# Performance work log

Hardware: AMD Instinct MI355X
Metric: run time of the kernel (lower is better)

Reference implementation:

```python
import jax, jax.numpy as jnp
import numpy as np

NUM_ITERATIONS = 5
NUM_TERMS = 3  # (degree + 1) // 2 with degree = 5
INITIAL_SCALE = 1.1


def setup_inputs() -> dict:
    key = jax.random.key(0)
    k1, k2 = jax.random.split(key)
    X = jax.random.normal(k1, (64, 1024, 1024), dtype=jnp.float32)
    coefficients = jnp.array([3.4445, -4.7750, 2.0315], dtype=jnp.float32)
    return {"X": X, "coefficients": coefficients}


def reference(X, coefficients):
    # Normalize each matrix to Frobenius norm INITIAL_SCALE
    fro = jnp.sqrt(jnp.sum(X * X, axis=(-2, -1), keepdims=True))
    X = X / fro * INITIAL_SCALE
    for _ in range(NUM_ITERATIONS):
        # XTX = X^T X, shape [B, M, M]
        XTX = jnp.einsum('bji,bjk->bik', X, X)
        term = X
        acc = coefficients[0] * X
        for i in range(1, NUM_TERMS):
            term = jnp.einsum('bij,bjk->bik', term, XTX)  # X (X^T X)^i
            acc = acc + coefficients[i] * term
        X = acc
    return X
```

## Files before the change

### kernel.cpp

```cpp
#include <hip/hip_runtime.h>
#include <hip/hip_bf16.h>
#include <stdint.h>

typedef float f32x4 __attribute__((ext_vector_type(4)));
typedef short bf16x8 __attribute__((ext_vector_type(8)));

#define LDW 1024
#define BATCH_SH 20

__device__ __forceinline__ float b2f(__hip_bfloat16 h) { return __bfloat162float(h); }
__device__ __forceinline__ __hip_bfloat16 f2b(float f) { return __float2bfloat16(f); }

__device__ __forceinline__ void gload16(const void* g, void* l) {
  __builtin_amdgcn_global_load_lds((const __attribute__((address_space(1))) void*)g,
                                   (__attribute__((address_space(3))) void*)l,
                                   16, 0, 0);
}

__global__ void k_partial(const float* __restrict__ xin, float* __restrict__ partials) {
  const int b = blockIdx.y, ch = blockIdx.x, t = threadIdx.x;
  const size_t base = ((size_t)b << BATCH_SH) + (size_t)ch * 16384;
  float s = 0.f;
#pragma unroll
  for (int i = 0; i < 16; ++i) {
    f32x4 v = *reinterpret_cast<const f32x4*>(xin + base + (size_t)(i * 256 + t) * 4);
    s += v[0] * v[0] + v[1] * v[1] + v[2] * v[2] + v[3] * v[3];
  }
#pragma unroll
  for (int off = 32; off; off >>= 1) s += __shfl_down(s, off);
  __shared__ float red[4];
  if ((t & 63) == 0) red[t >> 6] = s;
  __syncthreads();
  if (t == 0) partials[b * 64 + ch] = red[0] + red[1] + red[2] + red[3];
}

__global__ void k_scalesplit(const float* __restrict__ xin, const float* __restrict__ partials,
                             __hip_bfloat16* __restrict__ Xh, __hip_bfloat16* __restrict__ Xl,
                             __hip_bfloat16* __restrict__ XTh, __hip_bfloat16* __restrict__ XTl) {
  __shared__ float tile[64][65];
  const int b = blockIdx.z, tm = blockIdx.y, tn = blockIdx.x;
  const size_t boff = (size_t)b << BATCH_SH;
  const int t = threadIdx.x, lr0 = t >> 6, lc = t & 63;
  float q = partials[b * 64 + (t & 63)];
#pragma unroll
  for (int off = 32; off; off >>= 1) q += __shfl_down(q, off);
  q = __shfl(q, 0);
  const float s = 1.1f / sqrtf(q);
#pragma unroll
  for (int p = 0; p < 16; ++p) {
    const int lr = p * 4 + lr0;
    const size_t idx = boff + (size_t)(tm * 64 + lr) * LDW + tn * 64 + lc;
    const float v = xin[idx] * s;
    __hip_bfloat16 h = f2b(v);
    Xh[idx] = h;
    Xl[idx] = f2b(v - b2f(h));
    tile[lr][lc] = v;
  }
  __syncthreads();
#pragma unroll
  for (int p = 0; p < 16; ++p) {
    const int lr = p * 4 + lr0;
    const float v = tile[lc][lr];
    const size_t idx = boff + (size_t)(tn * 64 + lr) * LDW + tm * 64 + lc;
    __hip_bfloat16 h = f2b(v);
    XTh[idx] = h;
    XTl[idx] = f2b(v - b2f(h));
  }
}


#define SEGPTRS(S)                                                                        \
  const int seg_ = (S) >> 4, k0_ = ((S) & 15) << 6;                                       \
  const __hip_bfloat16* pa_ = seg_ == 0 ? pa0 : seg_ == 1 ? pa1 : pa2;                    \
  const __hip_bfloat16* pb_ = seg_ == 0 ? pb0 : seg_ == 1 ? pb1 : pb2;

#define STAGE_GL(DB, S)                                                                   \
  {                                                                                       \
    SEGPTRS(S)                                                                            \
    char* lb_ = smem + (DB) * 65536;                                                      \
    _Pragma("unroll") for (int it_ = 0; it_ < 4; ++it_) {                                 \
      const int r_ = it_ * 64 + w * 8 + (l >> 3);                                         \
      const int kx_ = k0_ + (((l & 7) ^ (l >> 3)) << 3);                                  \
      gload16(pa_ + boff + (size_t)(rowA + r_) * LDW + kx_,                               \
              lb_ + (it_ * 64 + w * 8) * 128 + l * 16);                                   \
      gload16(pb_ + boff + (size_t)(rowB + r_) * LDW + kx_,                               \
              lb_ + 32768 + (it_ * 64 + w * 8) * 128 + l * 16);                           \
    }                                                                                     \
  }

#define MFMA_PHASE(KK, BASE)                                                              \
  {                                                                                       \
    bf16x8 av[8], bv[4];                                                                  \
    _Pragma("unroll") for (int mi_ = 0; mi_ < 8; ++mi_)                                   \
        av[mi_] = *reinterpret_cast<const bf16x8*>(smem + (BASE) + offA[KK][mi_]);        \
    _Pragma("unroll") for (int ni_ = 0; ni_ < 4; ++ni_)                                   \
        bv[ni_] = *reinterpret_cast<const bf16x8*>(smem + (BASE) + offB[KK][ni_]);        \
    __builtin_amdgcn_s_setprio(1);                                                        \
    _Pragma("unroll") for (int mi_ = 0; mi_ < 8; ++mi_)                                   \
        _Pragma("unroll") for (int ni_ = 0; ni_ < 4; ++ni_)                               \
            acc[mi_][ni_] = __builtin_amdgcn_mfma_f32_16x16x32_bf16(                      \
                av[mi_], bv[ni_], acc[mi_][ni_], 0, 0, 0);                                \
    __builtin_amdgcn_s_setprio(0);                                                        \
  }

template <int MODE>
__global__ __launch_bounds__(512, 2) void k_gemm(
    const __hip_bfloat16* __restrict__ pa0, const __hip_bfloat16* __restrict__ pa1,
    const __hip_bfloat16* __restrict__ pa2, const __hip_bfloat16* __restrict__ pb0,
    const __hip_bfloat16* __restrict__ pb1, const __hip_bfloat16* __restrict__ pb2,
    __hip_bfloat16* oh, __hip_bfloat16* ol,
    __hip_bfloat16* oth, __hip_bfloat16* otl,
    float* __restrict__ of,
    const __hip_bfloat16* __restrict__ eh, const __hip_bfloat16* __restrict__ el,
    const float* __restrict__ coef) {
  __shared__ __align__(16) char smem[131072];
  const int t = threadIdx.x;
  const int w = t >> 6, l = t & 63;
  const int wr = w >> 2, wc = w & 3;

  const int nwg = gridDim.x, q = nwg >> 3, r8 = nwg & 7;
  const int xcd = blockIdx.x & 7, o = blockIdx.x >> 3;
  const int wgid = (xcd < r8 ? xcd * (q + 1) : r8 * (q + 1) + (xcd - r8) * q) + o;

  int bat, tm, tn;
  if constexpr (MODE == 3) {
    bat = wgid >> 4;
    const int tile = wgid & 15;
    tm = tile >> 2; tn = tile & 3;
  } else {
    bat = (int)((unsigned)wgid / 10u);
    const int tile = wgid - bat * 10;
    tm = (tile < 4) ? 0 : (tile < 7) ? 1 : (tile < 9) ? 2 : 3;
    tn = (tile < 4) ? tile : (tile < 7) ? (tile - 3) : (tile < 9) ? (tile - 5) : 3;
  }
  const size_t boff = (size_t)bat << BATCH_SH;
  const int rowA = tm * 256, rowB = tn * 256;

  f32x4 acc[8][4];
#pragma unroll
  for (int i = 0; i < 8; ++i)
#pragma unroll
    for (int j = 0; j < 4; ++j) acc[i][j] = (f32x4){0.f, 0.f, 0.f, 0.f};

  int offA[2][8], offB[2][4];
#pragma unroll
  for (int kk = 0; kk < 2; ++kk) {
    const int g = kk * 4 + (l >> 4);
#pragma unroll
    for (int mi = 0; mi < 8; ++mi) {
      const int rA = wr * 128 + mi * 16 + (l & 15);
      offA[kk][mi] = rA * 128 + ((g ^ (rA & 7)) << 4);
    }
#pragma unroll
    for (int ni = 0; ni < 4; ++ni) {
      const int rB = wc * 64 + ni * 16 + (l & 15);
      offB[kk][ni] = 32768 + rB * 128 + ((g ^ (rB & 7)) << 4);
    }
  }

  STAGE_GL(0, 0);
  asm volatile("s_waitcnt vmcnt(0)" ::: "memory");
  __builtin_amdgcn_sched_barrier(0);
  __builtin_amdgcn_s_barrier();
  __builtin_amdgcn_sched_barrier(0);

  for (int s = 0; s < 48; ++s) {
    const int base = (s & 1) * 65536;
    if (s + 1 < 48) STAGE_GL((s & 1) ^ 1, s + 1);
    __builtin_amdgcn_sched_barrier(0);
    MFMA_PHASE(0, base);
    MFMA_PHASE(1, base);
    asm volatile("s_waitcnt vmcnt(0) lgkmcnt(0)" ::: "memory");
    __builtin_amdgcn_sched_barrier(0);
    __builtin_amdgcn_s_barrier();
    __builtin_amdgcn_sched_barrier(0);
  }

  float c0 = 0.f, c1 = 0.f, c2 = 0.f;
  if constexpr (MODE == 2) { c0 = coef[0]; c1 = coef[1]; c2 = coef[2]; }
  const int r0 = tm * 256 + wr * 128 + ((l >> 4) << 2);
  const int cb = tn * 256 + wc * 64 + (l & 15);
#pragma unroll
  for (int mi = 0; mi < 8; ++mi) {
#pragma unroll
    for (int ni = 0; ni < 4; ++ni) {
      const int ccol = cb + ni * 16;
#pragma unroll
      for (int j = 0; j < 4; ++j) {
        const int rrow = r0 + mi * 16 + j;
        const size_t idx = boff + (size_t)rrow * LDW + ccol;
        float v = acc[mi][ni][j];
        if constexpr (MODE == 2)
          v = c2 * v + c1 * (b2f(eh[idx]) + b2f(el[idx])) + (rrow == ccol ? c0 : 0.f);
        __hip_bfloat16 h = f2b(v);
        __hip_bfloat16 lo = f2b(v - b2f(h));
        if constexpr (MODE == 3) {
          if (oh) { oh[idx] = h; ol[idx] = lo; }
          if (of) of[idx] = v;
        } else {
          oh[idx] = h; ol[idx] = lo;
          if (tm != tn) {
            const size_t tix = boff + (size_t)ccol * LDW + rrow;
            oth[tix] = h; otl[tix] = lo;
          }
        }
      }
    }
  }

  if constexpr (MODE == 3) {
    if (oth) {
      unsigned* tlds = reinterpret_cast<unsigned*>(smem);
      unsigned short* pth = reinterpret_cast<unsigned short*>(oth);
      unsigned short* ptl = reinterpret_cast<unsigned short*>(otl);
#pragma unroll
      for (int h2 = 0; h2 < 2; ++h2) {
        __builtin_amdgcn_s_barrier();
        if ((wc >> 1) == h2) {
#pragma unroll
          for (int mi = 0; mi < 8; ++mi) {
#pragma unroll
            for (int ni = 0; ni < 4; ++ni) {
              const int cl = (wc & 1) * 64 + ni * 16 + (l & 15);
#pragma unroll
              for (int j = 0; j < 4; ++j) {
                const int rr = wr * 128 + ((l >> 4) << 2) + mi * 16 + j;
                const float v = acc[mi][ni][j];
                const __hip_bfloat16 hh = f2b(v);
                const __hip_bfloat16 lo = f2b(v - b2f(hh));
                const unsigned pk = (unsigned)(*(const unsigned short*)&hh) |
                                    ((unsigned)(*(const unsigned short*)&lo) << 16);
                tlds[rr * 128 + (cl ^ ((rr >> 1) & 31))] = pk;
              }
            }
          }
        }
        __builtin_amdgcn_s_barrier();
#pragma unroll
        for (int i = 0; i < 16; ++i) {
          const int trow = w * 16 + i;
          const size_t obase =
              boff + (size_t)(tn * 256 + h2 * 128 + trow) * LDW + tm * 256;
#pragma unroll
          for (int c = 0; c < 2; ++c) {
            const int e0 = (c * 64 + l) * 2;
            const int m = (e0 >> 1) & 31;
            const unsigned p0 = tlds[e0 * 128 + (trow ^ m)];
            const unsigned p1 = tlds[(e0 + 1) * 128 + (trow ^ m)];
            *reinterpret_cast<unsigned*>(pth + obase + e0) =
                (p0 & 0xffffu) | (p1 << 16);
            *reinterpret_cast<unsigned*>(ptl + obase + e0) =
                (p0 >> 16) | (p1 & 0xffff0000u);
          }
        }
      }
    }
  }
}

extern "C" void kernel_launch(void* const* d_in, const int* in_sizes, int n_in,
                              void* d_out, int out_size, void* d_ws, size_t ws_size,
                              hipStream_t stream) {
  (void)in_sizes; (void)n_in; (void)out_size;
  const float* xin = (const float*)d_in[0];
  const float* coef = (const float*)d_in[1];
  float* xout = (float*)d_out;

  int CH = 64;
  while (CH > 1 && ((size_t)CH * 16u * 1024u * 1024u + 65536u) > ws_size) CH >>= 1;

  const size_t nE = (size_t)CH << BATCH_SH;
  __hip_bfloat16* P0h = (__hip_bfloat16*)d_ws;
  __hip_bfloat16* P0l = P0h + nE;
  __hip_bfloat16* P1h = P0l + nE;
  __hip_bfloat16* P1l = P1h + nE;
  __hip_bfloat16* P2h = P1l + nE;
  __hip_bfloat16* P2l = P2h + nE;
  __hip_bfloat16* XTh = P2l + nE;
  __hip_bfloat16* XTl = XTh + nE;
  float* partials = (float*)(XTl + nE);

  for (int c = 0; c < 64; c += CH) {
    const float* xi = xin + ((size_t)c << BATCH_SH);
    float* X = xout + ((size_t)c << BATCH_SH);
    k_partial<<<dim3(64, CH), 256, 0, stream>>>(xi, partials);
    k_scalesplit<<<dim3(16, 16, CH), 256, 0, stream>>>(xi, partials, P0h, P0l, XTh, XTl);

    __hip_bfloat16 *Xh = P0h, *Xl = P0l, *Ah = P1h, *Al = P1l, *Bh = P2h, *Bl = P2l;
    for (int it = 0; it < 5; ++it) {
      k_gemm<1><<<dim3(CH * 10), 512, 0, stream>>>(XTh, XTh, XTl, XTh, XTl, XTh,
                                                   Ah, Al, Ah, Al, nullptr,
                                                   nullptr, nullptr, nullptr);
      k_gemm<2><<<dim3(CH * 10), 512, 0, stream>>>(Ah, Ah, Al, Ah, Al, Ah,
                                                   Bh, Bl, Bh, Bl, nullptr,
                                                   Ah, Al, coef);
      k_gemm<3><<<dim3(CH * 16), 512, 0, stream>>>(Xh, Xh, Xl, Bh, Bl, Bh,
                                                   (it < 4) ? Ah : nullptr,
                                                   (it < 4) ? Al : nullptr,
                                                   (it < 4) ? XTh : nullptr,
                                                   (it < 4) ? XTl : nullptr,
                                                   (it == 4) ? X : nullptr,
                                                   nullptr, nullptr, nullptr);
      __hip_bfloat16 *th = Xh, *tl = Xl;
      Xh = Ah; Xl = Al;
      Ah = Bh; Al = Bl;
      Bh = th; Bl = tl;
    }
  }
}
```

Measured before the change: 7.440 ms.

## Fuse all stages into a persistent megakernel with grid barriers and per-XCD work stealing

Replaces the sequence of norm, scale/split and three GEMM kernel launches per iteration with one persistent kernel of 256 blocks. Stages are separated by atomic grid barriers, and symmetric-GEMM tiles are handed out through per-XCD atomic work-stealing counters. Batches are pinned to XCDs so their data stays in that XCD's L2. This removes launch gaps and tail effects between the 17 launches, but the kernel now runs at one block per CU (launch bounds 512,1), adds spin-barrier overhead, and relies on all 256 blocks being co-resident.

```diff
diff --git a/kernel.cpp b/kernel.cpp
--- a/kernel.cpp
+++ b/kernel.cpp
@@ -7,6 +7,8 @@
 
 #define LDW 1024
 #define BATCH_SH 20
+#define NBLK 256
+#define SCOPE __HIP_MEMORY_SCOPE_AGENT
 
 __device__ __forceinline__ float b2f(__hip_bfloat16 h) { return __bfloat162float(h); }
 __device__ __forceinline__ __hip_bfloat16 f2b(float f) { return __float2bfloat16(f); }
@@ -17,55 +19,19 @@
                                    16, 0, 0);
 }
 
-__global__ void k_partial(const float* __restrict__ xin, float* __restrict__ partials) {
-  const int b = blockIdx.y, ch = blockIdx.x, t = threadIdx.x;
-  const size_t base = ((size_t)b << BATCH_SH) + (size_t)ch * 16384;
-  float s = 0.f;
-#pragma unroll
-  for (int i = 0; i < 16; ++i) {
-    f32x4 v = *reinterpret_cast<const f32x4*>(xin + base + (size_t)(i * 256 + t) * 4);
-    s += v[0] * v[0] + v[1] * v[1] + v[2] * v[2] + v[3] * v[3];
-  }
-#pragma unroll
-  for (int off = 32; off; off >>= 1) s += __shfl_down(s, off);
-  __shared__ float red[4];
-  if ((t & 63) == 0) red[t >> 6] = s;
+__device__ __forceinline__ void grid_bar(int* cnt, int idx) {
   __syncthreads();
-  if (t == 0) partials[b * 64 + ch] = red[0] + red[1] + red[2] + red[3];
-}
-
-__global__ void k_scalesplit(const float* __restrict__ xin, const float* __restrict__ partials,
-                             __hip_bfloat16* __restrict__ Xh, __hip_bfloat16* __restrict__ Xl,
-                             __hip_bfloat16* __restrict__ XTh, __hip_bfloat16* __restrict__ XTl) {
-  __shared__ float tile[64][65];
-  const int b = blockIdx.z, tm = blockIdx.y, tn = blockIdx.x;
-  const size_t boff = (size_t)b << BATCH_SH;
-  const int t = threadIdx.x, lr0 = t >> 6, lc = t & 63;
-  float q = partials[b * 64 + (t & 63)];
-#pragma unroll
-  for (int off = 32; off; off >>= 1) q += __shfl_down(q, off);
-  q = __shfl(q, 0);
-  const float s = 1.1f / sqrtf(q);
-#pragma unroll
-  for (int p = 0; p < 16; ++p) {
-    const int lr = p * 4 + lr0;
-    const size_t idx = boff + (size_t)(tm * 64 + lr) * LDW + tn * 64 + lc;
-    const float v = xin[idx] * s;
-    __hip_bfloat16 h = f2b(v);
-    Xh[idx] = h;
-    Xl[idx] = f2b(v - b2f(h));
-    tile[lr][lc] = v;
+  if (threadIdx.x == 0) {
+    __hip_atomic_fetch_add(cnt, 1, __ATOMIC_ACQ_REL, SCOPE);
+    const int target = idx * NBLK;
+    while (__hip_atomic_load(cnt, __ATOMIC_ACQUIRE, SCOPE) < target)
+      __builtin_amdgcn_s_sleep(2);
   }
   __syncthreads();
-#pragma unroll
-  for (int p = 0; p < 16; ++p) {
-    const int lr = p * 4 + lr0;
-    const float v = tile[lc][lr];
-    const size_t idx = boff + (size_t)(tn * 64 + lr) * LDW + tm * 64 + lc;
-    __hip_bfloat16 h = f2b(v);
-    XTh[idx] = h;
-    XTl[idx] = f2b(v - b2f(h));
-  }
+}
+
+__global__ void k_zero(int* p, int n) {
+  if ((int)threadIdx.x < n) p[threadIdx.x] = 0;
 }
 
 
@@ -103,37 +69,17 @@
     __builtin_amdgcn_s_setprio(0);                                                        \
   }
 
-template <int MODE>
-__global__ __launch_bounds__(512, 2) void k_gemm(
-    const __hip_bfloat16* __restrict__ pa0, const __hip_bfloat16* __restrict__ pa1,
-    const __hip_bfloat16* __restrict__ pa2, const __hip_bfloat16* __restrict__ pb0,
-    const __hip_bfloat16* __restrict__ pb1, const __hip_bfloat16* __restrict__ pb2,
+__device__ __forceinline__ void gemm_tile(
+    const int mode, char* smem, const int t, const size_t boff,
+    const int tm, const int tn,
+    const __hip_bfloat16* pa0, const __hip_bfloat16* pa1, const __hip_bfloat16* pa2,
+    const __hip_bfloat16* pb0, const __hip_bfloat16* pb1, const __hip_bfloat16* pb2,
     __hip_bfloat16* oh, __hip_bfloat16* ol,
-    __hip_bfloat16* oth, __hip_bfloat16* otl,
-    float* __restrict__ of,
-    const __hip_bfloat16* __restrict__ eh, const __hip_bfloat16* __restrict__ el,
-    const float* __restrict__ coef) {
-  __shared__ __align__(16) char smem[131072];
-  const int t = threadIdx.x;
+    __hip_bfloat16* oth, __hip_bfloat16* otl, float* of,
+    const __hip_bfloat16* eh, const __hip_bfloat16* el,
+    const float c0, const float c1, const float c2) {
   const int w = t >> 6, l = t & 63;
   const int wr = w >> 2, wc = w & 3;
-
-  const int nwg = gridDim.x, q = nwg >> 3, r8 = nwg & 7;
-  const int xcd = blockIdx.x & 7, o = blockIdx.x >> 3;
-  const int wgid = (xcd < r8 ? xcd * (q + 1) : r8 * (q + 1) + (xcd - r8) * q) + o;
-
-  int bat, tm, tn;
-  if constexpr (MODE == 3) {
-    bat = wgid >> 4;
-    const int tile = wgid & 15;
-    tm = tile >> 2; tn = tile & 3;
-  } else {
-    bat = (int)((unsigned)wgid / 10u);
-    const int tile = wgid - bat * 10;
-    tm = (tile < 4) ? 0 : (tile < 7) ? 1 : (tile < 9) ? 2 : 3;
-    tn = (tile < 4) ? tile : (tile < 7) ? (tile - 3) : (tile < 9) ? (tile - 5) : 3;
-  }
-  const size_t boff = (size_t)bat << BATCH_SH;
   const int rowA = tm * 256, rowB = tn * 256;
 
   f32x4 acc[8][4];
@@ -176,8 +122,6 @@
     __builtin_amdgcn_sched_barrier(0);
   }
 
-  float c0 = 0.f, c1 = 0.f, c2 = 0.f;
-  if constexpr (MODE == 2) { c0 = coef[0]; c1 = coef[1]; c2 = coef[2]; }
   const int r0 = tm * 256 + wr * 128 + ((l >> 4) << 2);
   const int cb = tn * 256 + wc * 64 + (l & 15);
 #pragma unroll
@@ -190,11 +134,11 @@
         const int rrow = r0 + mi * 16 + j;
         const size_t idx = boff + (size_t)rrow * LDW + ccol;
         float v = acc[mi][ni][j];
-        if constexpr (MODE == 2)
+        if (mode == 2)
           v = c2 * v + c1 * (b2f(eh[idx]) + b2f(el[idx])) + (rrow == ccol ? c0 : 0.f);
         __hip_bfloat16 h = f2b(v);
         __hip_bfloat16 lo = f2b(v - b2f(h));
-        if constexpr (MODE == 3) {
+        if (mode == 3) {
           if (oh) { oh[idx] = h; ol[idx] = lo; }
           if (of) of[idx] = v;
         } else {
@@ -208,53 +152,198 @@
     }
   }
 
-  if constexpr (MODE == 3) {
-    if (oth) {
-      unsigned* tlds = reinterpret_cast<unsigned*>(smem);
-      unsigned short* pth = reinterpret_cast<unsigned short*>(oth);
-      unsigned short* ptl = reinterpret_cast<unsigned short*>(otl);
-#pragma unroll
-      for (int h2 = 0; h2 < 2; ++h2) {
-        __builtin_amdgcn_s_barrier();
-        if ((wc >> 1) == h2) {
-#pragma unroll
-          for (int mi = 0; mi < 8; ++mi) {
-#pragma unroll
-            for (int ni = 0; ni < 4; ++ni) {
-              const int cl = (wc & 1) * 64 + ni * 16 + (l & 15);
-#pragma unroll
-              for (int j = 0; j < 4; ++j) {
-                const int rr = wr * 128 + ((l >> 4) << 2) + mi * 16 + j;
-                const float v = acc[mi][ni][j];
-                const __hip_bfloat16 hh = f2b(v);
-                const __hip_bfloat16 lo = f2b(v - b2f(hh));
-                const unsigned pk = (unsigned)(*(const unsigned short*)&hh) |
-                                    ((unsigned)(*(const unsigned short*)&lo) << 16);
-                tlds[rr * 128 + (cl ^ ((rr >> 1) & 31))] = pk;
-              }
+  if (mode == 3 && oth) {
+    unsigned* tlds = reinterpret_cast<unsigned*>(smem);
+    unsigned short* pth = reinterpret_cast<unsigned short*>(oth);
+    unsigned short* ptl = reinterpret_cast<unsigned short*>(otl);
+#pragma unroll
+    for (int h2 = 0; h2 < 2; ++h2) {
+      __builtin_amdgcn_s_barrier();
+      if ((wc >> 1) == h2) {
+#pragma unroll
+        for (int mi = 0; mi < 8; ++mi) {
+#pragma unroll
+          for (int ni = 0; ni < 4; ++ni) {
+            const int cl = (wc & 1) * 64 + ni * 16 + (l & 15);
+#pragma unroll
+            for (int j = 0; j < 4; ++j) {
+              const int rr = wr * 128 + ((l >> 4) << 2) + mi * 16 + j;
+              const float v = acc[mi][ni][j];
+              const __hip_bfloat16 hh = f2b(v);
+              const __hip_bfloat16 lo = f2b(v - b2f(hh));
+              const unsigned pk = (unsigned)(*(const unsigned short*)&hh) |
+                                  ((unsigned)(*(const unsigned short*)&lo) << 16);
+              tlds[rr * 128 + (cl ^ ((rr >> 1) & 31))] = pk;
             }
           }
         }
-        __builtin_amdgcn_s_barrier();
-#pragma unroll
-        for (int i = 0; i < 16; ++i) {
-          const int trow = w * 16 + i;
-          const size_t obase =
-              boff + (size_t)(tn * 256 + h2 * 128 + trow) * LDW + tm * 256;
-#pragma unroll
-          for (int c = 0; c < 2; ++c) {
-            const int e0 = (c * 64 + l) * 2;
-            const int m = (e0 >> 1) & 31;
-            const unsigned p0 = tlds[e0 * 128 + (trow ^ m)];
-            const unsigned p1 = tlds[(e0 + 1) * 128 + (trow ^ m)];
-            *reinterpret_cast<unsigned*>(pth + obase + e0) =
-                (p0 & 0xffffu) | (p1 << 16);
-            *reinterpret_cast<unsigned*>(ptl + obase + e0) =
-                (p0 >> 16) | (p1 & 0xffff0000u);
-          }
+      }
+      __builtin_amdgcn_s_barrier();
+#pragma unroll
+      for (int i = 0; i < 16; ++i) {
+        const int trow = w * 16 + i;
+        const size_t obase = boff + (size_t)(tn * 256 + h2 * 128 + trow) * LDW + tm * 256;
+#pragma unroll
+        for (int c = 0; c < 2; ++c) {
+          const int e0 = (c * 64 + l) * 2;
+          const int m = (e0 >> 1) & 31;
+          const unsigned p0 = tlds[e0 * 128 + (trow ^ m)];
+          const unsigned p1 = tlds[(e0 + 1) * 128 + (trow ^ m)];
+          *reinterpret_cast<unsigned*>(pth + obase + e0) = (p0 & 0xffffu) | (p1 << 16);
+          *reinterpret_cast<unsigned*>(ptl + obase + e0) = (p0 >> 16) | (p1 & 0xffff0000u);
         }
       }
     }
+    __syncthreads();
+  }
+}
+
+__global__ __launch_bounds__(512, 1) void k_mega(
+    const float* __restrict__ xin, const float* __restrict__ coef,
+    float* __restrict__ xout,
+    __hip_bfloat16* P0h, __hip_bfloat16* P0l,
+    __hip_bfloat16* P1h, __hip_bfloat16* P1l,
+    __hip_bfloat16* P2h, __hip_bfloat16* P2l,
+    __hip_bfloat16* XTh, __hip_bfloat16* XTl,
+    float* __restrict__ partials, int* cnt, int* steal, const int CH) {
+  __shared__ __align__(16) char smem[131072];
+  __shared__ int jslot;
+  const int t = threadIdx.x, bid = blockIdx.x;
+  const int xcd = bid & 7, lid = bid >> 3;
+  const int bpx = CH >> 3;
+  int bar = 0;
+
+  {
+    const int per = CH * 8;
+    float* red = reinterpret_cast<float*>(smem);
+    for (int j = lid; j < per; j += 32) {
+      const int f = xcd * per + j;
+      const int b = f >> 6, ch = f & 63;
+      const size_t base = ((size_t)b << BATCH_SH) + (size_t)ch * 16384;
+      float s = 0.f;
+#pragma unroll
+      for (int i = 0; i < 8; ++i) {
+        f32x4 v = *reinterpret_cast<const f32x4*>(xin + base + (size_t)(i * 512 + t) * 4);
+        s += v[0] * v[0] + v[1] * v[1] + v[2] * v[2] + v[3] * v[3];
+      }
+#pragma unroll
+      for (int off = 32; off; off >>= 1) s += __shfl_down(s, off);
+      if ((t & 63) == 0) red[t >> 6] = s;
+      __syncthreads();
+      if (t == 0) {
+        float tot = 0.f;
+#pragma unroll
+        for (int i = 0; i < 8; ++i) tot += red[i];
+        partials[f] = tot;
+      }
+      __syncthreads();
+    }
+  }
+  grid_bar(cnt, ++bar);
+
+  {
+    const int per = CH * 32;
+    float* tile = reinterpret_cast<float*>(smem);
+    const int lr0 = t >> 6, lc = t & 63;
+    for (int j = lid; j < per; j += 32) {
+      const int f = xcd * per + j;
+      const int b = f >> 8, t256 = f & 255;
+      const int tmm = t256 >> 4, tnn = t256 & 15;
+      const size_t boff = (size_t)b << BATCH_SH;
+      float q = partials[b * 64 + (t & 63)];
+#pragma unroll
+      for (int off = 32; off; off >>= 1) q += __shfl_down(q, off);
+      q = __shfl(q, 0);
+      const float sc = 1.1f / sqrtf(q);
+#pragma unroll
+      for (int p = 0; p < 8; ++p) {
+        const int lr = p * 8 + lr0;
+        const size_t idx = boff + (size_t)(tmm * 64 + lr) * LDW + tnn * 64 + lc;
+        const float v = xin[idx] * sc;
+        __hip_bfloat16 h = f2b(v);
+        P0h[idx] = h;
+        P0l[idx] = f2b(v - b2f(h));
+        tile[lr * 65 + lc] = v;
+      }
+      __syncthreads();
+#pragma unroll
+      for (int p = 0; p < 8; ++p) {
+        const int lr = p * 8 + lr0;
+        const float v = tile[lc * 65 + lr];
+        const size_t idx = boff + (size_t)(tnn * 64 + lr) * LDW + tmm * 64 + lc;
+        __hip_bfloat16 h = f2b(v);
+        XTh[idx] = h;
+        XTl[idx] = f2b(v - b2f(h));
+      }
+      __syncthreads();
+    }
+  }
+  grid_bar(cnt, ++bar);
+
+  const float c0 = coef[0], c1 = coef[1], c2 = coef[2];
+
+  for (int it = 0; it < 5; ++it) {
+    const int rX = it % 3, rA = (it + 1) % 3, rB = (it + 2) % 3;
+    __hip_bfloat16* Xh = rX == 0 ? P0h : rX == 1 ? P1h : P2h;
+    __hip_bfloat16* Xl = rX == 0 ? P0l : rX == 1 ? P1l : P2l;
+    __hip_bfloat16* Ah = rA == 0 ? P0h : rA == 1 ? P1h : P2h;
+    __hip_bfloat16* Al = rA == 0 ? P0l : rA == 1 ? P1l : P2l;
+    __hip_bfloat16* Bh = rB == 0 ? P0h : rB == 1 ? P1h : P2h;
+    __hip_bfloat16* Bl = rB == 0 ? P0l : rB == 1 ? P1l : P2l;
+
+    {
+      const int NT = (CH * 10) >> 3;
+      int* ctr = steal + (it * 2) * 8 + xcd;
+      for (;;) {
+        if (t == 0) jslot = __hip_atomic_fetch_add(ctr, 1, __ATOMIC_RELAXED, SCOPE);
+        __syncthreads();
+        const int j = jslot;
+        __syncthreads();
+        if (j >= NT) break;
+        const int bat = xcd * bpx + j / 10;
+        const int tl = j - (j / 10) * 10;
+        const int tmm = (tl < 4) ? 0 : (tl < 7) ? 1 : (tl < 9) ? 2 : 3;
+        const int tnn = (tl < 4) ? tl : (tl < 7) ? (tl - 3) : (tl < 9) ? (tl - 5) : 3;
+        gemm_tile(1, smem, t, (size_t)bat << BATCH_SH, tmm, tnn,
+                  XTh, XTh, XTl, XTh, XTl, XTh,
+                  Ah, Al, Ah, Al, nullptr, nullptr, nullptr, 0.f, 0.f, 0.f);
+      }
+    }
+    grid_bar(cnt, ++bar);
+
+    {
+      const int NT = (CH * 10) >> 3;
+      int* ctr = steal + (it * 2 + 1) * 8 + xcd;
+      for (;;) {
+        if (t == 0) jslot = __hip_atomic_fetch_add(ctr, 1, __ATOMIC_RELAXED, SCOPE);
+        __syncthreads();
+        const int j = jslot;
+        __syncthreads();
+        if (j >= NT) break;
+        const int bat = xcd * bpx + j / 10;
+        const int tl = j - (j / 10) * 10;
+        const int tmm = (tl < 4) ? 0 : (tl < 7) ? 1 : (tl < 9) ? 2 : 3;
+        const int tnn = (tl < 4) ? tl : (tl < 7) ? (tl - 3) : (tl < 9) ? (tl - 5) : 3;
+        gemm_tile(2, smem, t, (size_t)bat << BATCH_SH, tmm, tnn,
+                  Ah, Ah, Al, Ah, Al, Ah,
+                  Bh, Bl, Bh, Bl, nullptr, Ah, Al, c0, c1, c2);
+      }
+    }
+    grid_bar(cnt, ++bar);
+
+    {
+      const int NT = CH * 2;
+      for (int j = lid; j < NT; j += 32) {
+        const int bat = xcd * bpx + (j >> 4);
+        const int t16 = j & 15;
+        gemm_tile(3, smem, t, (size_t)bat << BATCH_SH, t16 >> 2, t16 & 3,
+                  Xh, Xh, Xl, Bh, Bl, Bh,
+                  (it < 4) ? Ah : nullptr, (it < 4) ? Al : nullptr,
+                  (it < 4) ? XTh : nullptr, (it < 4) ? XTl : nullptr,
+                  (it == 4) ? xout : nullptr, nullptr, nullptr, 0.f, 0.f, 0.f);
+      }
+    }
+    if (it < 4) grid_bar(cnt, ++bar);
   }
 }
 
@@ -267,7 +356,7 @@
   float* xout = (float*)d_out;
 
   int CH = 64;
-  while (CH > 1 && ((size_t)CH * 16u * 1024u * 1024u + 65536u) > ws_size) CH >>= 1;
+  while (CH > 8 && ((size_t)CH * 16u * 1024u * 1024u + 65536u) > ws_size) CH >>= 1;
 
   const size_t nE = (size_t)CH << BATCH_SH;
   __hip_bfloat16* P0h = (__hip_bfloat16*)d_ws;
@@ -279,32 +368,14 @@
   __hip_bfloat16* XTh = P2l + nE;
   __hip_bfloat16* XTl = XTh + nE;
   float* partials = (float*)(XTl + nE);
+  int* sync_area = (int*)(partials + (size_t)CH * 64);
 
   for (int c = 0; c < 64; c += CH) {
     const float* xi = xin + ((size_t)c << BATCH_SH);
     float* X = xout + ((size_t)c << BATCH_SH);
-    k_partial<<<dim3(64, CH), 256, 0, stream>>>(xi, partials);
-    k_scalesplit<<<dim3(16, 16, CH), 256, 0, stream>>>(xi, partials, P0h, P0l, XTh, XTl);
-
-    __hip_bfloat16 *Xh = P0h, *Xl = P0l, *Ah = P1h, *Al = P1l, *Bh = P2h, *Bl = P2l;
-    for (int it = 0; it < 5; ++it) {
-      k_gemm<1><<<dim3(CH * 10), 512, 0, stream>>>(XTh, XTh, XTl, XTh, XTl, XTh,
-                                                   Ah, Al, Ah, Al, nullptr,
-                                                   nullptr, nullptr, nullptr);
-      k_gemm<2><<<dim3(CH * 10), 512, 0, stream>>>(Ah, Ah, Al, Ah, Al, Ah,
-                                                   Bh, Bl, Bh, Bl, nullptr,
-                                                   Ah, Al, coef);
-      k_gemm<3><<<dim3(CH * 16), 512, 0, stream>>>(Xh, Xh, Xl, Bh, Bl, Bh,
-                                                   (it < 4) ? Ah : nullptr,
-                                                   (it < 4) ? Al : nullptr,
-                                                   (it < 4) ? XTh : nullptr,
-                                                   (it < 4) ? XTl : nullptr,
-                                                   (it == 4) ? X : nullptr,
-                                                   nullptr, nullptr, nullptr);
-      __hip_bfloat16 *th = Xh, *tl = Xl;
-      Xh = Ah; Xl = Al;
-      Ah = Bh; Al = Bl;
-      Bh = th; Bl = tl;
-    }
-  }
-}
+    k_zero<<<dim3(1), 128, 0, stream>>>(sync_area, 81);
+    k_mega<<<dim3(NBLK), 512, 0, stream>>>(xi, coef, X,
+                                           P0h, P0l, P1h, P1l, P2h, P2l, XTh, XTl,
+                                           partials, sync_area, sync_area + 1, CH);
+  }
+}
```

New measurement: 27.74 ms. 273% more time.

## Prefetch two stages ahead and overlap global loads with second MFMA half

Applied to the files above, without the earlier changes.

Restructures the GEMM main loop so that two K-stages are in flight. Each iteration reads the second half's fragments into registers, then issues a barrier so the current buffer can be refilled with stage s+2 while the second MFMA half runs. It waits on vmcnt(8) instead of draining all loads, so global-load latency is hidden more deeply. The cost is more live registers for the extra fragments, plus an additional barrier per iteration.

```diff
diff --git a/kernel.cpp b/kernel.cpp
--- a/kernel.cpp
+++ b/kernel.cpp
@@ -88,20 +88,16 @@
     }                                                                                     \
   }
 
-#define MFMA_PHASE(KK, BASE)                                                              \
-  {                                                                                       \
-    bf16x8 av[8], bv[4];                                                                  \
-    _Pragma("unroll") for (int mi_ = 0; mi_ < 8; ++mi_)                                   \
-        av[mi_] = *reinterpret_cast<const bf16x8*>(smem + (BASE) + offA[KK][mi_]);        \
-    _Pragma("unroll") for (int ni_ = 0; ni_ < 4; ++ni_)                                   \
-        bv[ni_] = *reinterpret_cast<const bf16x8*>(smem + (BASE) + offB[KK][ni_]);        \
-    __builtin_amdgcn_s_setprio(1);                                                        \
-    _Pragma("unroll") for (int mi_ = 0; mi_ < 8; ++mi_)                                   \
-        _Pragma("unroll") for (int ni_ = 0; ni_ < 4; ++ni_)                               \
-            acc[mi_][ni_] = __builtin_amdgcn_mfma_f32_16x16x32_bf16(                      \
-                av[mi_], bv[ni_], acc[mi_][ni_], 0, 0, 0);                                \
-    __builtin_amdgcn_s_setprio(0);                                                        \
-  }
+#define MFMA_CL(AV, BV)                                                                   \
+  __builtin_amdgcn_s_setprio(1);                                                          \
+  _Pragma("unroll") for (int mi_ = 0; mi_ < 8; ++mi_)                                     \
+      _Pragma("unroll") for (int ni_ = 0; ni_ < 4; ++ni_)                                 \
+          acc[mi_][ni_] = __builtin_amdgcn_mfma_f32_16x16x32_bf16(                        \
+              AV[mi_], BV[ni_], acc[mi_][ni_], 0, 0, 0);                                  \
+  __builtin_amdgcn_s_setprio(0);
+
+#define SCB() __builtin_amdgcn_sched_barrier(0)
+#define BAR() __builtin_amdgcn_s_barrier()
 
 template <int MODE>
 __global__ __launch_bounds__(512, 2) void k_gemm(
@@ -159,21 +155,43 @@
   }
 
   STAGE_GL(0, 0);
-  asm volatile("s_waitcnt vmcnt(0)" ::: "memory");
-  __builtin_amdgcn_sched_barrier(0);
-  __builtin_amdgcn_s_barrier();
-  __builtin_amdgcn_sched_barrier(0);
+  STAGE_GL(1, 1);
+  asm volatile("s_waitcnt vmcnt(8)" ::: "memory");
+  SCB();
+  BAR();
+  SCB();
 
   for (int s = 0; s < 48; ++s) {
     const int base = (s & 1) * 65536;
-    if (s + 1 < 48) STAGE_GL((s & 1) ^ 1, s + 1);
-    __builtin_amdgcn_sched_barrier(0);
-    MFMA_PHASE(0, base);
-    MFMA_PHASE(1, base);
-    asm volatile("s_waitcnt vmcnt(0) lgkmcnt(0)" ::: "memory");
-    __builtin_amdgcn_sched_barrier(0);
-    __builtin_amdgcn_s_barrier();
-    __builtin_amdgcn_sched_barrier(0);
+    bf16x8 av0[8], bv0[4], av1[8], bv1[4];
+#pragma unroll
+    for (int i = 0; i < 8; ++i)
+      av0[i] = *reinterpret_cast<const bf16x8*>(smem + base + offA[0][i]);
+#pragma unroll
+    for (int i = 0; i < 4; ++i)
+      bv0[i] = *reinterpret_cast<const bf16x8*>(smem + base + offB[0][i]);
+    MFMA_CL(av0, bv0);
+#pragma unroll
+    for (int i = 0; i < 8; ++i)
+      av1[i] = *reinterpret_cast<const bf16x8*>(smem + base + offA[1][i]);
+#pragma unroll
+    for (int i = 0; i < 4; ++i)
+      bv1[i] = *reinterpret_cast<const bf16x8*>(smem + base + offB[1][i]);
+    asm volatile("s_waitcnt lgkmcnt(0)" ::: "memory");
+    SCB();
+    BAR();
+    SCB();
+    if (s + 2 < 48) STAGE_GL((s & 1), s + 2);
+    SCB();
+    MFMA_CL(av1, bv1);
+    if (s + 2 < 48) {
+      asm volatile("s_waitcnt vmcnt(8)" ::: "memory");
+    } else {
+      asm volatile("s_waitcnt vmcnt(0)" ::: "memory");
+    }
+    SCB();
+    BAR();
+    SCB();
   }
 
   float c0 = 0.f, c1 = 0.f, c2 = 0.f;
```

After: 7.542 ms. Within noise of the previous version (+1.4%).
